# Performance work log

Measured on AMD Instinct MI355X. Metric: run time of the kernel, lower is better.

Reference implementation:

```python
import jax, jax.numpy as jnp
import numpy as np


def _count_components(img, cls):
    """Count 4-connected components of pixels equal to `cls` in a 2D int map.

    Equivalent to the numba DFS flood fill: each component is counted once.
    Implemented as min-label propagation: seed every in-class pixel with its
    linear index, iterate min over 4-neighbors (same-class only, since
    out-of-class pixels hold the sentinel BIG) until convergence; a component
    root is a pixel whose final label equals its own index.
    """
    H, W = img.shape
    BIG = H * W  # sentinel larger than any pixel index
    mask = img == cls
    idx = jnp.arange(BIG, dtype=jnp.int32).reshape(H, W)
    lab0 = jnp.where(mask, idx, BIG).astype(jnp.int32)

    def cond(state):
        return state[1]

    def body(state):
        lab, _ = state
        p = jnp.pad(lab, 1, constant_values=BIG)
        nmin = jnp.minimum(jnp.minimum(p[:-2, 1:-1], p[2:, 1:-1]),
                           jnp.minimum(p[1:-1, :-2], p[1:-1, 2:]))
        new = jnp.where(mask, jnp.minimum(lab, nmin), BIG)
        return new, jnp.any(new != lab)

    lab, _ = jax.lax.while_loop(cond, body, (lab0, jnp.array(True)))
    # roots: in-class pixels whose propagated label is their own index
    return jnp.sum(mask & (lab == idx)).astype(jnp.float32)


def _counts23(img):
    # component counts for labels 2 and 3 (the only ones the loss uses)
    return _count_components(img, 2), _count_components(img, 3)


def setup_inputs() -> dict:
    key = jax.random.key(0)
    k1, k2 = jax.random.split(key)
    pred = jax.random.normal(k1, (8, 4, 1, 768, 768), dtype=jnp.float32)
    anno = jax.random.randint(k2, (8, 1, 768, 768), 0, 4, dtype=jnp.int32)
    return {"pred": pred, "anno": anno}


def reference(pred, anno):
    # pred: [B, C, 1, H, W], anno: [B, 1, H, W]
    pred_argmax = jnp.argmax(pred, axis=1)[:, 0]  # [B, H, W] (detached semantics)
    anno_map = anno[:, 0]                          # [B, H, W]
    a2, a3 = jax.vmap(_counts23)(anno_map)
    p2, p3 = jax.vmap(_counts23)(pred_argmax)
    term2 = 1.0 - 2.0 * jnp.minimum(p2, a2) / (a2 + p2)
    term3 = 1.0 - 2.0 * jnp.minimum(p3, a3) / (a3 + p3)
    # original sums per-batch terms into connEF, then loss = connEF / 2
    return jnp.sum(term2 + term3) / 2.0
```

## Files before the change

### kernel.cpp

```cpp
#include <hip/hip_runtime.h>

#define W     768
#define PIX   (768*768)
#define NMAPS 16
#define TROWS 6
#define TPX   (TROWS*W)
#define NT    (768/TROWS)
#define NB    (NT-1)
#define NSEG  (TPX/64)
#define NIT   (NSEG/4)
#define CSLOT 16


__device__ __forceinline__ int find_root_p(volatile int* L, int x) {
    int y = L[x] >> 2;
    while (y != x) { x = y; y = L[x] >> 2; }
    return x;
}

__device__ __forceinline__ void unite_p(int* L, int a, int b, int c) {
    volatile int* Lv = L;
    while (true) {
        a = find_root_p(Lv, a);
        b = find_root_p(Lv, b);
        if (a == b) return;
        if (a > b) { int t = a; a = b; b = t; }
        int old = atomicMin(&L[b], (a << 2) | c);
        if ((old >> 2) == b) return;
        b = old >> 2;
    }
}

__device__ __forceinline__ bool unite_gp(int* L, int a, int b, int c) {
    volatile int* Lv = L;
    while (true) {
        a = find_root_p(Lv, a);
        b = find_root_p(Lv, b);
        if (a == b) return false;
        if (a > b) { int t = a; a = b; b = t; }
        int old = atomicMin(&L[b], (a << 2) | c);
        if ((old >> 2) == b) return true;
        b = old >> 2;
    }
}


__global__ __launch_bounds__(256) void fused_k(const float* __restrict__ pred,
                                               const int*   __restrict__ anno,
                                               int* __restrict__ labels,
                                               int* __restrict__ counts, int m0) {
    __shared__ int lab[TPX];
    __shared__ int s2[4], s3[4];

    int mc   = blockIdx.x / NT;
    int t    = blockIdx.x - mc * NT;
    int m    = m0 + mc;
    int tid  = threadIdx.x;
    int wid  = tid >> 6;
    int lane = tid & 63;

    int pc[3] = {0, 0, 0};
    int pm[3] = {0, 0, 0};

    const int*   asrc = anno + (size_t)m * PIX + (size_t)t * TPX;
    const float* psrc = pred + (size_t)(m < 8 ? 0 : (m - 8)) * 4 * PIX + (size_t)t * TPX;
    bool is_anno = (m < 8);

    #pragma unroll
    for (int it = 0; it < NIT; ++it) {
        int seg = wid + 4 * it;
        int px  = seg * 64 + lane;
        int c;
        if (is_anno) {
            c = asrc[px] & 3;
        } else {
            float v0 = psrc[px];
            float v1 = psrc[(size_t)PIX + px];
            float v2 = psrc[(size_t)2 * PIX + px];
            float v3 = psrc[(size_t)3 * PIX + px];
            c = 0; float bv = v0;
            if (v1 > bv) { bv = v1; c = 1; }
            if (v2 > bv) { bv = v2; c = 2; }
            if (v3 > bv) { bv = v3; c = 3; }
        }
        int cl = __shfl_up(c, 1);
        unsigned long long bm = __ballot(lane == 0 || c != cl);
        int ms = 63 - __clzll(bm & ((2ULL << lane) - 1));
        lab[px] = ((seg * 64 + ms) << 2) | c;
        const int sl = it % 3;
        if (it >= 3) {
            if ((c & 2) && c == pc[sl]) {
                int mx = ms > pm[sl] ? ms : pm[sl];
                if (lane == mx) unite_p(lab, px - W, px, c);
            }
        }
        pc[sl] = c; pm[sl] = ms;
    }
    __syncthreads();

    if (tid < TROWS * 11) {
        int row = tid / 11, j = tid % 11;
        int px  = row * W + (j + 1) * 64;
        int v = lab[px], c = v & 3;
        if (c & 2) {
            int vl = lab[px - 1];
            if ((vl & 3) == c) unite_p(lab, px - 1, px, c);
        }
    }
    __syncthreads();

    int c2 = 0, c3 = 0;
    int lbase = t * TPX;
    int* gl = labels + (size_t)mc * PIX + lbase;
    #pragma unroll
    for (int it = 0; it < NIT; ++it) {
        int seg = wid + 4 * it;
        int px  = seg * 64 + lane;
        int v   = lab[px];
        int c   = v & 3;
        bool incls  = (c & 2) != 0;
        bool isroot = incls && ((v >> 2) == px);
        if (isroot) { if (c == 2) c2++; else c3++; }
        if (it < 3 || it >= NIT - 3) {
            int outv;
            if (incls) {
                int r = find_root_p(lab, px);
                outv = ((lbase + r) << 2) | c;
            } else {
                outv = ((lbase + px) << 2) | c;
            }
            gl[px] = outv;
        } else if (isroot) {
            gl[px] = ((lbase + px) << 2) | c;
        }
    }
    for (int off = 32; off; off >>= 1) {
        c2 += __shfl_down(c2, off, 64);
        c3 += __shfl_down(c3, off, 64);
    }
    if (lane == 0) { s2[wid] = c2; s3[wid] = c3; }
    __syncthreads();
    if (tid == 0) {
        int t2 = s2[0] + s2[1] + s2[2] + s2[3];
        int t3 = s3[0] + s3[1] + s3[2] + s3[3];
        if (t2) atomicAdd(&counts[(m * 2 + 0) * CSLOT], t2);
        if (t3) atomicAdd(&counts[(m * 2 + 1) * CSLOT], t3);
    }
}

__global__ __launch_bounds__(256) void boundary_k(int* __restrict__ labels,
                                                  int* __restrict__ counts, int m0) {
    __shared__ int s2[4], s3[4];
    const int HM = NB * (W / 2);
    int i    = blockIdx.x * 256 + threadIdx.x;
    int mc   = blockIdx.y;
    int m    = m0 + mc;
    int lane = threadIdx.x & 63;

    int m2 = 0, m3 = 0;
    if (i < HM) {
        int b   = i / (W / 2);
        int col = (i - b * (W / 2)) * 2;
        int* L  = labels + (size_t)mc * PIX;
        int p1  = b * TPX + (TROWS - 1) * W + col;
        int p2  = p1 + W;
        int2 va = *(const int2*)&L[p1];
        int2 vb = *(const int2*)&L[p2];
        int pay = __shfl_up(va.y, 1), pby = __shfl_up(vb.y, 1);
        int c0 = va.x & 3;
        if (c0 == (vb.x & 3) && (c0 & 2)) {
            bool red = (lane > 0) && (pay == va.x) && (pby == vb.x);
            if (!red && unite_gp(L, p1, p2, c0)) { if (c0 == 2) m2++; else m3++; }
        }
        int c1 = va.y & 3;
        if (c1 == (vb.y & 3) && (c1 & 2)) {
            bool red = (va.x == va.y) && (vb.x == vb.y);
            if (!red && unite_gp(L, p1 + 1, p2 + 1, c1)) { if (c1 == 2) m2++; else m3++; }
        }
    }
    for (int off = 32; off; off >>= 1) {
        m2 += __shfl_down(m2, off, 64);
        m3 += __shfl_down(m3, off, 64);
    }
    int wid = threadIdx.x >> 6;
    if (lane == 0) { s2[wid] = m2; s3[wid] = m3; }
    __syncthreads();
    if (threadIdx.x == 0) {
        int t2 = s2[0] + s2[1] + s2[2] + s2[3];
        int t3 = s3[0] + s3[1] + s3[2] + s3[3];
        if (t2) atomicSub(&counts[(m * 2 + 0) * CSLOT], t2);
        if (t3) atomicSub(&counts[(m * 2 + 1) * CSLOT], t3);
    }
}

__global__ void final_k(const int* __restrict__ counts, float* __restrict__ out) {
    float s = 0.0f;
    for (int b = 0; b < 8; ++b) {
        float a2 = (float)counts[(b * 2 + 0) * CSLOT];
        float a3 = (float)counts[(b * 2 + 1) * CSLOT];
        float p2 = (float)counts[((8 + b) * 2 + 0) * CSLOT];
        float p3 = (float)counts[((8 + b) * 2 + 1) * CSLOT];
        float t2 = 1.0f - 2.0f * fminf(p2, a2) / (a2 + p2);
        float t3 = 1.0f - 2.0f * fminf(p3, a3) / (a3 + p3);
        s += t2 + t3;
    }
    out[0] = 0.5f * s;
}


extern "C" void kernel_launch(void* const* d_in, const int* in_sizes, int n_in,
                              void* d_out, int out_size, void* d_ws, size_t ws_size,
                              hipStream_t stream) {
    const float* pred = (const float*)d_in[0];
    const int*   anno = (const int*)d_in[1];
    float* out = (float*)d_out;

    int* counts = (int*)d_ws;
    char* base  = (char*)d_ws + 4096;

    const size_t per_map = (size_t)PIX * 4;
    size_t avail = (ws_size > 4096) ? ws_size - 4096 : 0;
    int K = (int)(avail / per_map);
    if (K > NMAPS) K = NMAPS;
    if (K < 1)     K = 1;

    hipMemsetAsync(counts, 0, 32 * CSLOT * sizeof(int), stream);

    const int HM = NB * (W / 2);
    for (int m0 = 0; m0 < NMAPS; m0 += K) {
        int nm = NMAPS - m0; if (nm > K) nm = K;
        int* labels = (int*)base;
        fused_k   <<<dim3(nm * NT), 256, 0, stream>>>(pred, anno, labels, counts, m0);
        boundary_k<<<dim3((HM + 255) / 256, nm), 256, 0, stream>>>(labels, counts, m0);
    }
    final_k<<<1, 1, 0, stream>>>(counts, out);
}
```

Baseline: 59.01 us.

## Process 4 pixels per thread with 256-wide strips and vectorized loads

Restructures the tile scan so each of 192 threads handles 4 consecutive pixels per row, with each wave owning a 256-pixel strip across the 6 rows. Loads and LDS/global stores become 128-bit vectors, and run-start detection uses four ballots combined per lane. The change also cuts the horizontal seam fixups from 66 to 12 per tile. It aims to reduce instruction count and memory transactions per pixel, at the cost of more registers and more union-find work per thread.

Measured after the change: 66.37 us. 1.12x slower.

```diff
diff --git a/kernel.cpp b/kernel.cpp
--- a/kernel.cpp
+++ b/kernel.cpp
@@ -7,8 +7,7 @@
 #define TPX   (TROWS*W)
 #define NT    (768/TROWS)
 #define NB    (NT-1)
-#define NSEG  (TPX/64)
-#define NIT   (NSEG/4)
+#define STRIP 256
 #define CSLOT 16
 
 
@@ -45,62 +44,97 @@
 }
 
 
-__global__ __launch_bounds__(256) void fused_k(const float* __restrict__ pred,
-                                               const int*   __restrict__ anno,
-                                               int* __restrict__ labels,
-                                               int* __restrict__ counts, int m0) {
+__global__ __launch_bounds__(192, 6) void fused_k(const float* __restrict__ pred,
+                                                  const int*   __restrict__ anno,
+                                                  int* __restrict__ labels,
+                                                  int* __restrict__ counts, int m0) {
     __shared__ int lab[TPX];
-    __shared__ int s2[4], s3[4];
+    __shared__ int s2[3], s3[3];
 
     int mc   = blockIdx.x / NT;
     int t    = blockIdx.x - mc * NT;
     int m    = m0 + mc;
     int tid  = threadIdx.x;
-    int wid  = tid >> 6;
+    int wid  = tid / 64;
     int lane = tid & 63;
-
-    int pc[3] = {0, 0, 0};
-    int pm[3] = {0, 0, 0};
+    int p    = lane * 4;
+
+    unsigned long long ltm = (1ULL << lane) - 1;
+    unsigned long long lem = ltm | (1ULL << lane);
 
     const int*   asrc = anno + (size_t)m * PIX + (size_t)t * TPX;
     const float* psrc = pred + (size_t)(m < 8 ? 0 : (m - 8)) * 4 * PIX + (size_t)t * TPX;
     bool is_anno = (m < 8);
 
+    int pcc = 0, prs = 0;
+
     #pragma unroll
-    for (int it = 0; it < NIT; ++it) {
-        int seg = wid + 4 * it;
-        int px  = seg * 64 + lane;
-        int c;
+    for (int r = 0; r < TROWS; ++r) {
+        int base = r * W + wid * STRIP;
+        int px0  = base + p;
+        int c0, c1, c2, c3;
         if (is_anno) {
-            c = asrc[px] & 3;
+            int4 v = *(const int4*)&asrc[px0];
+            c0 = v.x & 3; c1 = v.y & 3; c2 = v.z & 3; c3 = v.w & 3;
         } else {
-            float v0 = psrc[px];
-            float v1 = psrc[(size_t)PIX + px];
-            float v2 = psrc[(size_t)2 * PIX + px];
-            float v3 = psrc[(size_t)3 * PIX + px];
-            c = 0; float bv = v0;
-            if (v1 > bv) { bv = v1; c = 1; }
-            if (v2 > bv) { bv = v2; c = 2; }
-            if (v3 > bv) { bv = v3; c = 3; }
-        }
-        int cl = __shfl_up(c, 1);
-        unsigned long long bm = __ballot(lane == 0 || c != cl);
-        int ms = 63 - __clzll(bm & ((2ULL << lane) - 1));
-        lab[px] = ((seg * 64 + ms) << 2) | c;
-        const int sl = it % 3;
-        if (it >= 3) {
-            if ((c & 2) && c == pc[sl]) {
-                int mx = ms > pm[sl] ? ms : pm[sl];
-                if (lane == mx) unite_p(lab, px - W, px, c);
-            }
-        }
-        pc[sl] = c; pm[sl] = ms;
-    }
-    __syncthreads();
-
-    if (tid < TROWS * 11) {
-        int row = tid / 11, j = tid % 11;
-        int px  = row * W + (j + 1) * 64;
+            const float4* f = (const float4*)psrc;
+            int i4 = px0 >> 2;
+            float4 v0 = f[i4];
+            float4 v1 = f[(PIX >> 2) + i4];
+            float4 v2 = f[2 * (PIX >> 2) + i4];
+            float4 v3 = f[3 * (PIX >> 2) + i4];
+            {   float bv = v0.x; c0 = 0;
+                if (v1.x > bv) { bv = v1.x; c0 = 1; }
+                if (v2.x > bv) { bv = v2.x; c0 = 2; }
+                if (v3.x > bv) { bv = v3.x; c0 = 3; } }
+            {   float bv = v0.y; c1 = 0;
+                if (v1.y > bv) { bv = v1.y; c1 = 1; }
+                if (v2.y > bv) { bv = v2.y; c1 = 2; }
+                if (v3.y > bv) { bv = v3.y; c1 = 3; } }
+            {   float bv = v0.z; c2 = 0;
+                if (v1.z > bv) { bv = v1.z; c2 = 1; }
+                if (v2.z > bv) { bv = v2.z; c2 = 2; }
+                if (v3.z > bv) { bv = v3.z; c2 = 3; } }
+            {   float bv = v0.w; c3 = 0;
+                if (v1.w > bv) { bv = v1.w; c3 = 1; }
+                if (v2.w > bv) { bv = v2.w; c3 = 2; }
+                if (v3.w > bv) { bv = v3.w; c3 = 3; } }
+        }
+        int prev3 = __shfl_up(c3, 1);
+        bool sf0 = (lane == 0) || (c0 != prev3);
+        bool sf1 = (c1 != c0), sf2 = (c2 != c1), sf3 = (c3 != c2);
+        unsigned long long b0 = __ballot(sf0);
+        unsigned long long b1 = __ballot(sf1);
+        unsigned long long b2 = __ballot(sf2);
+        unsigned long long b3 = __ballot(sf3);
+        int rs0 = (63 - __clzll(b0 & lem)) * 4;
+        unsigned long long mm;
+        mm = b1 & ltm; if (mm) { int q = (63 - __clzll(mm)) * 4 + 1; if (q > rs0) rs0 = q; }
+        mm = b2 & ltm; if (mm) { int q = (63 - __clzll(mm)) * 4 + 2; if (q > rs0) rs0 = q; }
+        mm = b3 & ltm; if (mm) { int q = (63 - __clzll(mm)) * 4 + 3; if (q > rs0) rs0 = q; }
+        int rs1 = sf1 ? p + 1 : rs0;
+        int rs2 = sf2 ? p + 2 : rs1;
+        int rs3 = sf3 ? p + 3 : rs2;
+        int lb  = (base << 2);
+        int4 ov = make_int4(lb + (rs0 << 2) + c0, lb + (rs1 << 2) + c1,
+                            lb + (rs2 << 2) + c2, lb + (rs3 << 2) + c3);
+        *(int4*)&lab[px0] = ov;
+        if (r > 0) {
+            int pc0 = pcc & 3, pc1 = (pcc >> 2) & 3, pc2 = (pcc >> 4) & 3, pc3 = (pcc >> 6) & 3;
+            int pr0 = prs & 255, pr1 = (prs >> 8) & 255, pr2 = (prs >> 16) & 255, pr3 = (prs >> 24) & 255;
+            if ((c0 & 2) && c0 == pc0) { int mx = rs0 > pr0 ? rs0 : pr0; if (mx == p)     unite_p(lab, px0 - W,     px0,     c0); }
+            if ((c1 & 2) && c1 == pc1) { int mx = rs1 > pr1 ? rs1 : pr1; if (mx == p + 1) unite_p(lab, px0 + 1 - W, px0 + 1, c1); }
+            if ((c2 & 2) && c2 == pc2) { int mx = rs2 > pr2 ? rs2 : pr2; if (mx == p + 2) unite_p(lab, px0 + 2 - W, px0 + 2, c2); }
+            if ((c3 & 2) && c3 == pc3) { int mx = rs3 > pr3 ? rs3 : pr3; if (mx == p + 3) unite_p(lab, px0 + 3 - W, px0 + 3, c3); }
+        }
+        pcc = c0 | (c1 << 2) | (c2 << 4) | (c3 << 6);
+        prs = rs0 | (rs1 << 8) | (rs2 << 16) | (rs3 << 24);
+    }
+    __syncthreads();
+
+    if (tid < TROWS * 2) {
+        int row = tid >> 1, s = (tid & 1) + 1;
+        int px  = row * W + s * STRIP;
         int v = lab[px], c = v & 3;
         if (c & 2) {
             int vl = lab[px - 1];
@@ -109,40 +143,45 @@
     }
     __syncthreads();
 
-    int c2 = 0, c3 = 0;
+    int n2 = 0, n3 = 0;
     int lbase = t * TPX;
     int* gl = labels + (size_t)mc * PIX + lbase;
     #pragma unroll
-    for (int it = 0; it < NIT; ++it) {
-        int seg = wid + 4 * it;
-        int px  = seg * 64 + lane;
-        int v   = lab[px];
-        int c   = v & 3;
-        bool incls  = (c & 2) != 0;
-        bool isroot = incls && ((v >> 2) == px);
-        if (isroot) { if (c == 2) c2++; else c3++; }
-        if (it < 3 || it >= NIT - 3) {
-            int outv;
-            if (incls) {
-                int r = find_root_p(lab, px);
-                outv = ((lbase + r) << 2) | c;
-            } else {
-                outv = ((lbase + px) << 2) | c;
-            }
-            gl[px] = outv;
-        } else if (isroot) {
-            gl[px] = ((lbase + px) << 2) | c;
+    for (int r = 0; r < TROWS; ++r) {
+        int px0 = r * W + wid * STRIP + p;
+        int4 v = *(int4*)&lab[px0];
+        int c0 = v.x & 3, c1 = v.y & 3, c2 = v.z & 3, c3 = v.w & 3;
+        bool r0 = (c0 & 2) && (v.x >> 2) == px0;
+        bool r1 = (c1 & 2) && (v.y >> 2) == px0 + 1;
+        bool r2 = (c2 & 2) && (v.z >> 2) == px0 + 2;
+        bool r3 = (c3 & 2) && (v.w >> 2) == px0 + 3;
+        if (r0) { if (c0 == 2) n2++; else n3++; }
+        if (r1) { if (c1 == 2) n2++; else n3++; }
+        if (r2) { if (c2 == 2) n2++; else n3++; }
+        if (r3) { if (c3 == 2) n2++; else n3++; }
+        if (r == 0 || r == TROWS - 1) {
+            int4 ov;
+            ov.x = (c0 & 2) ? (((lbase + find_root_p(lab, px0    )) << 2) | c0) : (((lbase + px0    ) << 2) | c0);
+            ov.y = (c1 & 2) ? (((lbase + find_root_p(lab, px0 + 1)) << 2) | c1) : (((lbase + px0 + 1) << 2) | c1);
+            ov.z = (c2 & 2) ? (((lbase + find_root_p(lab, px0 + 2)) << 2) | c2) : (((lbase + px0 + 2) << 2) | c2);
+            ov.w = (c3 & 2) ? (((lbase + find_root_p(lab, px0 + 3)) << 2) | c3) : (((lbase + px0 + 3) << 2) | c3);
+            *(int4*)&gl[px0] = ov;
+        } else {
+            if (r0) gl[px0]     = ((lbase + px0)     << 2) | c0;
+            if (r1) gl[px0 + 1] = ((lbase + px0 + 1) << 2) | c1;
+            if (r2) gl[px0 + 2] = ((lbase + px0 + 2) << 2) | c2;
+            if (r3) gl[px0 + 3] = ((lbase + px0 + 3) << 2) | c3;
         }
     }
     for (int off = 32; off; off >>= 1) {
-        c2 += __shfl_down(c2, off, 64);
-        c3 += __shfl_down(c3, off, 64);
-    }
-    if (lane == 0) { s2[wid] = c2; s3[wid] = c3; }
+        n2 += __shfl_down(n2, off, 64);
+        n3 += __shfl_down(n3, off, 64);
+    }
+    if (lane == 0) { s2[wid] = n2; s3[wid] = n3; }
     __syncthreads();
     if (tid == 0) {
-        int t2 = s2[0] + s2[1] + s2[2] + s2[3];
-        int t3 = s3[0] + s3[1] + s3[2] + s3[3];
+        int t2 = s2[0] + s2[1] + s2[2];
+        int t3 = s3[0] + s3[1] + s3[2];
         if (t2) atomicAdd(&counts[(m * 2 + 0) * CSLOT], t2);
         if (t3) atomicAdd(&counts[(m * 2 + 1) * CSLOT], t3);
     }
@@ -230,7 +269,7 @@
     for (int m0 = 0; m0 < NMAPS; m0 += K) {
         int nm = NMAPS - m0; if (nm > K) nm = K;
         int* labels = (int*)base;
-        fused_k   <<<dim3(nm * NT), 256, 0, stream>>>(pred, anno, labels, counts, m0);
+        fused_k   <<<dim3(nm * NT), 192, 0, stream>>>(pred, anno, labels, counts, m0);
         boundary_k<<<dim3((HM + 255) / 256, nm), 256, 0, stream>>>(labels, counts, m0);
     }
     final_k<<<1, 1, 0, stream>>>(counts, out);
```
